# Kernel tuning notes

Hardware: AMD Instinct MI355X
Metric: run time of the kernel (lower is better)

## Reference

```python
import jax, jax.numpy as jnp
import numpy as np

# Config (Qwen3-4B-like, from ModelConfig defaults in source)
B = 32          # batch = number of decode requests = total_q
H = 32          # num_attention_heads
KVH = 8         # num_key_value_heads
G = H // KVH    # num_kv_groups = 4
D = 128         # head_dim
HID = 2560      # hidden_size
PS = 16         # page_size
MAXP = 128      # max_num_pages per request
NPAGES = B * MAXP   # 4096 pages in pool
MAXKV = MAXP * PS   # 2048
THETA = 5000000.0
EPS = 1e-6


def setup_inputs() -> dict:
    key = jax.random.key(0)
    ks = jax.random.split(key, 12)
    x = jax.random.normal(ks[0], (1, B, HID), dtype=jnp.float32)
    Wq = jax.random.normal(ks[1], (H * D, HID), dtype=jnp.float32) * 0.02
    Wk = jax.random.normal(ks[2], (KVH * D, HID), dtype=jnp.float32) * 0.02
    Wv = jax.random.normal(ks[3], (KVH * D, HID), dtype=jnp.float32) * 0.02
    Wo = jax.random.normal(ks[4], (HID, H * D), dtype=jnp.float32) * 0.02
    q_norm_w = jnp.ones((D,), dtype=jnp.float32)
    k_norm_w = jnp.ones((D,), dtype=jnp.float32)
    K_pool = jax.random.normal(ks[5], (NPAGES, PS, KVH, D), dtype=jnp.float32) * 0.02
    V_pool = jax.random.normal(ks[6], (NPAGES, PS, KVH, D), dtype=jnp.float32) * 0.02
    # each request owns a disjoint contiguous run of pages
    page_indices = jnp.arange(NPAGES, dtype=jnp.int32).reshape(B, MAXP)
    # KV length AFTER writing the single new decode token, in [128, MAXKV]
    lengths_after = jax.random.randint(ks[7], (B,), 128, MAXKV + 1).astype(jnp.int32)
    pos = lengths_after - 1                                  # position of new token
    page_of = page_indices[jnp.arange(B), pos // PS]         # page holding it
    slot_mapping = page_of.astype(jnp.int64) * PS + (pos % PS).astype(jnp.int64)
    # RoPE tables at the new-token positions: cos/sin (1, total_q, 1, D)
    inv_freq = 1.0 / (THETA ** (jnp.arange(0, D, 2, dtype=jnp.float32) / D))
    ang = pos.astype(jnp.float32)[:, None] * inv_freq[None, :]   # (B, D/2)
    ang = jnp.concatenate([ang, ang], axis=-1)                   # (B, D)
    cos = jnp.cos(ang)[None, :, None, :]
    sin = jnp.sin(ang)[None, :, None, :]
    return {"x": x, "cos": cos, "sin": sin, "Wq": Wq, "Wk": Wk, "Wv": Wv,
            "Wo": Wo, "q_norm_w": q_norm_w, "k_norm_w": k_norm_w,
            "K_pool": K_pool, "V_pool": V_pool, "page_indices": page_indices,
            "lengths_after": lengths_after, "slot_mapping": slot_mapping}


def _rmsnorm(x, w):
    xf = x.astype(jnp.float32)
    xf = xf * jax.lax.rsqrt(jnp.mean(xf * xf, axis=-1, keepdims=True) + EPS)
    return (w * xf).astype(x.dtype)


def _rope(x, cos, sin):
    # x: (1, heads, S, D); cos/sin: (1, S, 1, D) -> (1, 1, S, D)
    c = jnp.swapaxes(cos, 1, 2).astype(x.dtype)
    s = jnp.swapaxes(sin, 1, 2).astype(x.dtype)
    x1, x2 = jnp.split(x, 2, axis=-1)
    rot = jnp.concatenate([-x2, x1], axis=-1)
    return x * c + rot * s


def reference(x, cos, sin, Wq, Wk, Wv, Wo, q_norm_w, k_norm_w,
              K_pool, V_pool, page_indices, lengths_after, slot_mapping):
    total_q = x.shape[1]  # == B for decode
    # projections -> (1, heads, total_q, D)
    q = jnp.einsum('bsh,oh->bso', x, Wq).reshape(1, total_q, H, D).transpose(0, 2, 1, 3)
    k = jnp.einsum('bsh,oh->bso', x, Wk).reshape(1, total_q, KVH, D).transpose(0, 2, 1, 3)
    v = jnp.einsum('bsh,oh->bso', x, Wv).reshape(1, total_q, KVH, D).transpose(0, 2, 1, 3)
    # QK-norm (per-head RMSNorm on head_dim), then RoPE
    q = _rope(_rmsnorm(q, q_norm_w), cos, sin)
    k = _rope(_rmsnorm(k, k_norm_w), cos, sin)
    # write new K/V into the page pool (index_copy_ equivalent)
    k_pack = jnp.swapaxes(k[0], 0, 1)  # (total_q, KVH, D)
    v_pack = jnp.swapaxes(v[0], 0, 1)
    Kf = K_pool.reshape(NPAGES * PS, KVH, D).at[slot_mapping].set(k_pack)
    Vf = V_pool.reshape(NPAGES * PS, KVH, D).at[slot_mapping].set(v_pack)
    Kp = Kf.reshape(NPAGES, PS, KVH, D)
    Vp = Vf.reshape(NPAGES, PS, KVH, D)
    # decode path: full page-table gather per request
    flat_idx = page_indices.reshape(-1)
    k_all = Kp[flat_idx].reshape(B, MAXKV, KVH, D)
    v_all = Vp[flat_idx].reshape(B, MAXKV, KVH, D)
    # GQA attention, single query per request; scale = 1/sqrt(D) (SDPA default)
    qg = jnp.swapaxes(q[0], 0, 1).reshape(B, KVH, G, D)  # (B, KVH, G, D)
    scores = jnp.einsum('bkgd,bskd->bkgs', qg, k_all) * (1.0 / np.sqrt(D))
    invalid = jnp.arange(MAXKV)[None, :] >= lengths_after[:, None]  # (B, MAXKV)
    scores = jnp.where(invalid[:, None, None, :], -jnp.inf, scores)
    probs = jax.nn.softmax(scores, axis=-1)
    out = jnp.einsum('bkgs,bskd->bkgd', probs, v_all).reshape(B, H * D)
    y = jnp.einsum('bo,ho->bh', out, Wo)  # o_proj
    return y[None]  # (1, total_q, HID)
```

## Files before the change

kernel.cpp:

```cpp
#include <hip/hip_runtime.h>
#include <math.h>

#define NB    32
#define HIDV  2560
#define HD    128
#define NQH   32
#define NKVH  8

typedef __bf16 bf16x8 __attribute__((ext_vector_type(8)));
typedef float  f32x4  __attribute__((ext_vector_type(4)));

__device__ __forceinline__ unsigned bfpack(float a, float b) {
  unsigned ua = __float_as_uint(a), ub = __float_as_uint(b);
  ua = (ua + 0x7FFFu + ((ua >> 16) & 1u)) >> 16;
  ub = (ub + 0x7FFFu + ((ub >> 16) & 1u)) >> 16;
  return ua | (ub << 16);
}

__device__ __forceinline__ void gemm_body(
    const float* __restrict__ X, const float* __restrict__ W,
    float* __restrict__ P, int N, int K, int f0, int kc, int t,
    unsigned short* Wl, unsigned short* Xl) {
  const float* Wg = W + (size_t)f0 * K + (size_t)kc * 256;
  #pragma unroll
  for (int i = 0; i < 16; ++i) {
    int idx = i * 256 + t;
    int row = idx >> 6, c4 = idx & 63;
    float4 w4 = *(const float4*)(Wg + (size_t)row * K + c4 * 4);
    *(uint2*)((char*)Wl + row * 528 + c4 * 8) =
        make_uint2(bfpack(w4.x, w4.y), bfpack(w4.z, w4.w));
  }
  const float* Xg = X + (size_t)kc * 256;
  #pragma unroll
  for (int i = 0; i < 8; ++i) {
    int idx = i * 256 + t;
    int row = idx >> 6, c4 = idx & 63;
    float4 x4 = *(const float4*)(Xg + (size_t)row * K + c4 * 4);
    *(uint2*)((char*)Xl + row * 528 + c4 * 8) =
        make_uint2(bfpack(x4.x, x4.y), bfpack(x4.z, x4.w));
  }
  __syncthreads();

  const int w = t >> 6, l = t & 63;
  const int rA = l & 15, kq = l >> 4;
  f32x4 acc0 = {0.f, 0.f, 0.f, 0.f}, acc1 = {0.f, 0.f, 0.f, 0.f};
  const char* pa0 = (const char*)Xl + rA * 528 + kq * 16;
  const char* pa1 = pa0 + 16 * 528;
  const char* pb  = (const char*)Wl + (w * 16 + rA) * 528 + kq * 16;
  #pragma unroll
  for (int ks = 0; ks < 8; ++ks) {
    bf16x8 a0 = *(const bf16x8*)(pa0 + ks * 64);
    bf16x8 a1 = *(const bf16x8*)(pa1 + ks * 64);
    bf16x8 bb = *(const bf16x8*)(pb  + ks * 64);
    acc0 = __builtin_amdgcn_mfma_f32_16x16x32_bf16(a0, bb, acc0, 0, 0, 0);
    acc1 = __builtin_amdgcn_mfma_f32_16x16x32_bf16(a1, bb, acc1, 0, 0, 0);
  }
  const int fcol = f0 + w * 16 + rA;
  float* Pr = P + ((size_t)kc * 32) * N + fcol;
  #pragma unroll
  for (int j = 0; j < 4; ++j) {
    int b0 = kq * 4 + j;
    Pr[(size_t)b0 * N]        = acc0[j];
    Pr[(size_t)(b0 + 16) * N] = acc1[j];
  }
}

__global__ __launch_bounds__(256) void qkv_gemm(
    const float* __restrict__ X, const float* __restrict__ Wq,
    const float* __restrict__ Wk, const float* __restrict__ Wv,
    float* __restrict__ qp, float* __restrict__ kp, float* __restrict__ vp) {
  __shared__ __align__(16) unsigned short Wl[64 * 264];
  __shared__ __align__(16) unsigned short Xl[32 * 264];
  const int bx = blockIdx.x;
  const float* W; float* P; int N, f0;
  if (bx < 64)      { W = Wq; P = qp; N = 4096; f0 = bx * 64; }
  else if (bx < 80) { W = Wk; P = kp; N = 1024; f0 = (bx - 64) * 64; }
  else              { W = Wv; P = vp; N = 1024; f0 = (bx - 80) * 64; }
  gemm_body(X, W, P, N, 2560, f0, blockIdx.y, threadIdx.x, Wl, Xl);
}

__global__ __launch_bounds__(256) void o_gemm(
    const float* __restrict__ X, const float* __restrict__ W,
    float* __restrict__ P) {
  __shared__ __align__(16) unsigned short Wl[64 * 264];
  __shared__ __align__(16) unsigned short Xl[32 * 264];
  gemm_body(X, W, P, 2560, 4096, blockIdx.x * 64, blockIdx.y, threadIdx.x, Wl, Xl);
}

__global__ __launch_bounds__(128) void finqkv(
    const float* __restrict__ qp, const float* __restrict__ kp,
    const float* __restrict__ vp, const float* __restrict__ cosb,
    const float* __restrict__ sinb, const float* __restrict__ qw,
    const float* __restrict__ kw, float* __restrict__ qn,
    float* __restrict__ kn, float* __restrict__ vn) {
  const int b = blockIdx.x, h = blockIdx.y, d = threadIdx.x;
  float x = 0.f;
  if (h < 32) {
    #pragma unroll
    for (int c = 0; c < 10; ++c) x += qp[(size_t)(c * 32 + b) * 4096 + h * 128 + d];
  } else if (h < 40) {
    #pragma unroll
    for (int c = 0; c < 10; ++c) x += kp[(size_t)(c * 32 + b) * 1024 + (h - 32) * 128 + d];
  } else {
    #pragma unroll
    for (int c = 0; c < 10; ++c) x += vp[(size_t)(c * 32 + b) * 1024 + (h - 40) * 128 + d];
  }
  if (h >= 40) { vn[((size_t)b * 8 + (h - 40)) * 128 + d] = x; return; }

  __shared__ float red[2];
  __shared__ float sh[128];
  float ss = x * x;
  #pragma unroll
  for (int mk = 1; mk < 64; mk <<= 1) ss += __shfl_xor(ss, mk);
  if ((d & 63) == 0) red[d >> 6] = ss;
  __syncthreads();
  const float inv = rsqrtf((red[0] + red[1]) * (1.f / 128.f) + 1e-6f);
  const float* nw = (h < 32) ? qw : kw;
  const float xn = x * inv * nw[d];
  sh[d] = xn;
  __syncthreads();
  const float rot = (d < 64) ? -sh[d + 64] : sh[d - 64];
  const float o = xn * cosb[b * 128 + d] + rot * sinb[b * 128 + d];
  if (h < 32) qn[((size_t)b * 32 + h) * 128 + d] = o;
  else        kn[((size_t)b * 8 + (h - 32)) * 128 + d] = o;
}

__global__ __launch_bounds__(512) void attn(
    const float* __restrict__ Kp, const float* __restrict__ Vp,
    const float* __restrict__ qn, const float* __restrict__ kn,
    const float* __restrict__ vn, const int* __restrict__ pidx,
    const int* __restrict__ lens, float* __restrict__ ao) {
  const int b = blockIdx.x >> 3, kvh = blockIdx.x & 7;
  const int t = threadIdx.x, w = t >> 6, l = t & 63;
  const int sub = l >> 4, di = (l & 15) * 8;
  __shared__ int pages[128];
  __shared__ float mmS[32][4], msS[32][4];
  __shared__ __align__(16) float maccS[32][4][128];
  if (t < 128) pages[t] = pidx[b * 128 + t];
  __syncthreads();
  const int len = lens[b], lim = len - 1;

  float qf[4][8];
  const float SC = 0.08838834764831845f * 1.4426950408889634f;
  #pragma unroll
  for (int g = 0; g < 4; ++g)
    #pragma unroll
    for (int j = 0; j < 8; ++j)
      qf[g][j] = qn[((size_t)b * 32 + kvh * 4 + g) * 128 + di + j] * SC;

  float m[4], se[4], acc[4][8];
  #pragma unroll
  for (int g = 0; g < 4; ++g) {
    m[g] = -INFINITY; se[g] = 0.f;
    #pragma unroll
    for (int j = 0; j < 8; ++j) acc[g][j] = 0.f;
  }

  const int t0 = w * 4 + sub;
  const int nit = (lim + 31) >> 5;

  auto update = [&](const float (&ck)[8], const float (&cv)[8], bool valid) {
    float s[4];
    #pragma unroll
    for (int g = 0; g < 4; ++g) {
      float d8 = 0.f;
      #pragma unroll
      for (int j = 0; j < 8; ++j) d8 += qf[g][j] * ck[j];
      s[g] = d8;
    }
    #pragma unroll
    for (int mk = 1; mk < 16; mk <<= 1) {
      #pragma unroll
      for (int g = 0; g < 4; ++g) s[g] += __shfl_xor(s[g], mk);
    }
    if (valid) {
      #pragma unroll
      for (int g = 0; g < 4; ++g) {
        const float sg = s[g];
        if (sg > m[g]) {
          const float scf = exp2f(m[g] - sg);
          m[g] = sg;
          se[g] = se[g] * scf + 1.f;
          #pragma unroll
          for (int j = 0; j < 8; ++j) acc[g][j] = acc[g][j] * scf + cv[j];
        } else {
          const float p = exp2f(sg - m[g]);
          se[g] += p;
          #pragma unroll
          for (int j = 0; j < 8; ++j) acc[g][j] += p * cv[j];
        }
      }
    }
  };

  f32x4 ka0, ka1, va0, va1, kb0, kb1, vb0, vb1;
  {
    int tt = min(t0, lim - 1);
    size_t a = ((size_t)pages[tt >> 4] * 16 + (tt & 15)) * 1024 + kvh * 128 + di;
    ka0 = *(const f32x4*)(Kp + a); ka1 = *(const f32x4*)(Kp + a + 4);
    va0 = *(const f32x4*)(Vp + a); va1 = *(const f32x4*)(Vp + a + 4);
  }
  if (nit > 1) {
    int tt = min(32 + t0, lim - 1);
    size_t a = ((size_t)pages[tt >> 4] * 16 + (tt & 15)) * 1024 + kvh * 128 + di;
    kb0 = *(const f32x4*)(Kp + a); kb1 = *(const f32x4*)(Kp + a + 4);
    vb0 = *(const f32x4*)(Vp + a); vb1 = *(const f32x4*)(Vp + a + 4);
  }
  for (int it = 0; it < nit; it += 2) {
    {
      const float ck[8] = {ka0[0], ka0[1], ka0[2], ka0[3], ka1[0], ka1[1], ka1[2], ka1[3]};
      const float cv[8] = {va0[0], va0[1], va0[2], va0[3], va1[0], va1[1], va1[2], va1[3]};
      if (it + 2 < nit) {
        int tt = min((it + 2) * 32 + t0, lim - 1);
        size_t a = ((size_t)pages[tt >> 4] * 16 + (tt & 15)) * 1024 + kvh * 128 + di;
        ka0 = *(const f32x4*)(Kp + a); ka1 = *(const f32x4*)(Kp + a + 4);
        va0 = *(const f32x4*)(Vp + a); va1 = *(const f32x4*)(Vp + a + 4);
      }
      update(ck, cv, it * 32 + t0 < lim);
    }
    if (it + 1 < nit) {
      const float ck[8] = {kb0[0], kb0[1], kb0[2], kb0[3], kb1[0], kb1[1], kb1[2], kb1[3]};
      const float cv[8] = {vb0[0], vb0[1], vb0[2], vb0[3], vb1[0], vb1[1], vb1[2], vb1[3]};
      if (it + 3 < nit) {
        int tt = min((it + 3) * 32 + t0, lim - 1);
        size_t a = ((size_t)pages[tt >> 4] * 16 + (tt & 15)) * 1024 + kvh * 128 + di;
        kb0 = *(const f32x4*)(Kp + a); kb1 = *(const f32x4*)(Kp + a + 4);
        vb0 = *(const f32x4*)(Vp + a); vb1 = *(const f32x4*)(Vp + a + 4);
      }
      update(ck, cv, (it + 1) * 32 + t0 < lim);
    }
  }

  if (w == 0) {
    const float* kr = kn + ((size_t)b * 8 + kvh) * 128 + di;
    const float* vr = vn + ((size_t)b * 8 + kvh) * 128 + di;
    float ck[8], cv[8];
    #pragma unroll
    for (int j = 0; j < 8; ++j) { ck[j] = kr[j]; cv[j] = vr[j]; }
    update(ck, cv, sub == 0);
  }

  const int st = w * 4 + sub;
  if ((l & 15) == 0) {
    #pragma unroll
    for (int g = 0; g < 4; ++g) { mmS[st][g] = m[g]; msS[st][g] = se[g]; }
  }
  #pragma unroll
  for (int g = 0; g < 4; ++g)
    #pragma unroll
    for (int j = 0; j < 8; ++j) maccS[st][g][di + j] = acc[g][j];
  __syncthreads();

  const int g = t >> 7, dd = t & 127;
  float M = -INFINITY;
  #pragma unroll
  for (int s2 = 0; s2 < 32; ++s2) M = fmaxf(M, mmS[s2][g]);
  float den = 0.f, num = 0.f;
  for (int s2 = 0; s2 < 32; ++s2) {
    const float wg = exp2f(mmS[s2][g] - M);
    den += wg * msS[s2][g];
    num += wg * maccS[s2][g][dd];
  }
  ao[((size_t)b * 32 + kvh * 4 + g) * 128 + dd] = num / den;
}

__global__ __launch_bounds__(256) void oreduce(const float* __restrict__ op,
                                               float* __restrict__ y) {
  const int i = blockIdx.x * 256 + threadIdx.x;
  float s = 0.f;
  #pragma unroll
  for (int c = 0; c < 16; ++c) s += op[(size_t)c * (32 * 2560) + i];
  y[i] = s;
}

extern "C" void kernel_launch(void* const* d_in, const int* in_sizes, int n_in,
                              void* d_out, int out_size, void* d_ws, size_t ws_size,
                              hipStream_t stream) {
  const float* x    = (const float*)d_in[0];
  const float* cosb = (const float*)d_in[1];
  const float* sinb = (const float*)d_in[2];
  const float* Wq   = (const float*)d_in[3];
  const float* Wk   = (const float*)d_in[4];
  const float* Wv   = (const float*)d_in[5];
  const float* Wo   = (const float*)d_in[6];
  const float* qw   = (const float*)d_in[7];
  const float* kw   = (const float*)d_in[8];
  const float* Kp   = (const float*)d_in[9];
  const float* Vp   = (const float*)d_in[10];
  const int*   pidx = (const int*)d_in[11];
  const int*   lens = (const int*)d_in[12];
  float* y = (float*)d_out;

  float* ws = (float*)d_ws;
  float* qp = ws;
  float* kp = qp + 1310720;
  float* vp = kp + 327680;
  float* qn = vp + 327680;
  float* kn = qn + 131072;
  float* vn = kn + 32768;
  float* ao = vn + 32768;
  float* op = qp;
  (void)in_sizes; (void)n_in; (void)out_size; (void)ws_size;

  qkv_gemm<<<dim3(96, 10), 256, 0, stream>>>(x, Wq, Wk, Wv, qp, kp, vp);
  finqkv<<<dim3(32, 48), 128, 0, stream>>>(qp, kp, vp, cosb, sinb, qw, kw, qn, kn, vn);
  attn<<<256, 512, 0, stream>>>(Kp, Vp, qn, kn, vn, pidx, lens, ao);
  o_gemm<<<dim3(40, 16), 256, 0, stream>>>(ao, Wo, op);
  oreduce<<<320, 256, 0, stream>>>(op, y);
}
```

Measured before the change: 99.00 us.

## Drop split-K in projection GEMMs and deepen attention KV prefetch

The QKV and output-projection GEMMs now loop over all K slabs inside one block instead of splitting K across the grid. This removes the partial-sum buffers, the separate oreduce kernel and the 10-way summation in finqkv. The attention loop now keeps four KV tiles in flight instead of two, to hide more load latency. In exchange the GEMM grids shrink to 96 and 40 blocks, far fewer than the number of CUs. Each block also streams its weight slabs serially with a barrier between them, so weight-bandwidth utilization may drop sharply.

```diff
diff --git a/kernel.cpp b/kernel.cpp
--- a/kernel.cpp
+++ b/kernel.cpp
@@ -19,44 +19,48 @@
 
 __device__ __forceinline__ void gemm_body(
     const float* __restrict__ X, const float* __restrict__ W,
-    float* __restrict__ P, int N, int K, int f0, int kc, int t,
+    float* __restrict__ P, int N, int K, int f0, int slabs, int t,
     unsigned short* Wl, unsigned short* Xl) {
-  const float* Wg = W + (size_t)f0 * K + (size_t)kc * 256;
-  #pragma unroll
-  for (int i = 0; i < 16; ++i) {
-    int idx = i * 256 + t;
-    int row = idx >> 6, c4 = idx & 63;
-    float4 w4 = *(const float4*)(Wg + (size_t)row * K + c4 * 4);
-    *(uint2*)((char*)Wl + row * 528 + c4 * 8) =
-        make_uint2(bfpack(w4.x, w4.y), bfpack(w4.z, w4.w));
-  }
-  const float* Xg = X + (size_t)kc * 256;
-  #pragma unroll
-  for (int i = 0; i < 8; ++i) {
-    int idx = i * 256 + t;
-    int row = idx >> 6, c4 = idx & 63;
-    float4 x4 = *(const float4*)(Xg + (size_t)row * K + c4 * 4);
-    *(uint2*)((char*)Xl + row * 528 + c4 * 8) =
-        make_uint2(bfpack(x4.x, x4.y), bfpack(x4.z, x4.w));
-  }
-  __syncthreads();
-
   const int w = t >> 6, l = t & 63;
   const int rA = l & 15, kq = l >> 4;
   f32x4 acc0 = {0.f, 0.f, 0.f, 0.f}, acc1 = {0.f, 0.f, 0.f, 0.f};
-  const char* pa0 = (const char*)Xl + rA * 528 + kq * 16;
-  const char* pa1 = pa0 + 16 * 528;
-  const char* pb  = (const char*)Wl + (w * 16 + rA) * 528 + kq * 16;
-  #pragma unroll
-  for (int ks = 0; ks < 8; ++ks) {
-    bf16x8 a0 = *(const bf16x8*)(pa0 + ks * 64);
-    bf16x8 a1 = *(const bf16x8*)(pa1 + ks * 64);
-    bf16x8 bb = *(const bf16x8*)(pb  + ks * 64);
-    acc0 = __builtin_amdgcn_mfma_f32_16x16x32_bf16(a0, bb, acc0, 0, 0, 0);
-    acc1 = __builtin_amdgcn_mfma_f32_16x16x32_bf16(a1, bb, acc1, 0, 0, 0);
+
+  for (int s = 0; s < slabs; ++s) {
+    if (s) __syncthreads();
+    const float* Wg = W + (size_t)f0 * K + (size_t)s * 256;
+    #pragma unroll
+    for (int i = 0; i < 16; ++i) {
+      int idx = i * 256 + t;
+      int row = idx >> 6, c4 = idx & 63;
+      float4 w4 = *(const float4*)(Wg + (size_t)row * K + c4 * 4);
+      *(uint2*)((char*)Wl + row * 528 + c4 * 8) =
+          make_uint2(bfpack(w4.x, w4.y), bfpack(w4.z, w4.w));
+    }
+    const float* Xg = X + (size_t)s * 256;
+    #pragma unroll
+    for (int i = 0; i < 8; ++i) {
+      int idx = i * 256 + t;
+      int row = idx >> 6, c4 = idx & 63;
+      float4 x4 = *(const float4*)(Xg + (size_t)row * K + c4 * 4);
+      *(uint2*)((char*)Xl + row * 528 + c4 * 8) =
+          make_uint2(bfpack(x4.x, x4.y), bfpack(x4.z, x4.w));
+    }
+    __syncthreads();
+
+    const char* pa0 = (const char*)Xl + rA * 528 + kq * 16;
+    const char* pa1 = pa0 + 16 * 528;
+    const char* pb  = (const char*)Wl + (w * 16 + rA) * 528 + kq * 16;
+    #pragma unroll
+    for (int ks = 0; ks < 8; ++ks) {
+      bf16x8 a0 = *(const bf16x8*)(pa0 + ks * 64);
+      bf16x8 a1 = *(const bf16x8*)(pa1 + ks * 64);
+      bf16x8 bb = *(const bf16x8*)(pb  + ks * 64);
+      acc0 = __builtin_amdgcn_mfma_f32_16x16x32_bf16(a0, bb, acc0, 0, 0, 0);
+      acc1 = __builtin_amdgcn_mfma_f32_16x16x32_bf16(a1, bb, acc1, 0, 0, 0);
+    }
   }
   const int fcol = f0 + w * 16 + rA;
-  float* Pr = P + ((size_t)kc * 32) * N + fcol;
+  float* Pr = P + fcol;
   #pragma unroll
   for (int j = 0; j < 4; ++j) {
     int b0 = kq * 4 + j;
@@ -76,15 +80,15 @@
   if (bx < 64)      { W = Wq; P = qp; N = 4096; f0 = bx * 64; }
   else if (bx < 80) { W = Wk; P = kp; N = 1024; f0 = (bx - 64) * 64; }
   else              { W = Wv; P = vp; N = 1024; f0 = (bx - 80) * 64; }
-  gemm_body(X, W, P, N, 2560, f0, blockIdx.y, threadIdx.x, Wl, Xl);
+  gemm_body(X, W, P, N, 2560, f0, 10, threadIdx.x, Wl, Xl);
 }
 
 __global__ __launch_bounds__(256) void o_gemm(
     const float* __restrict__ X, const float* __restrict__ W,
-    float* __restrict__ P) {
+    float* __restrict__ y) {
   __shared__ __align__(16) unsigned short Wl[64 * 264];
   __shared__ __align__(16) unsigned short Xl[32 * 264];
-  gemm_body(X, W, P, 2560, 4096, blockIdx.x * 64, blockIdx.y, threadIdx.x, Wl, Xl);
+  gemm_body(X, W, y, 2560, 4096, blockIdx.x * 64, 16, threadIdx.x, Wl, Xl);
 }
 
 __global__ __launch_bounds__(128) void finqkv(
@@ -94,17 +98,10 @@
     const float* __restrict__ kw, float* __restrict__ qn,
     float* __restrict__ kn, float* __restrict__ vn) {
   const int b = blockIdx.x, h = blockIdx.y, d = threadIdx.x;
-  float x = 0.f;
-  if (h < 32) {
-    #pragma unroll
-    for (int c = 0; c < 10; ++c) x += qp[(size_t)(c * 32 + b) * 4096 + h * 128 + d];
-  } else if (h < 40) {
-    #pragma unroll
-    for (int c = 0; c < 10; ++c) x += kp[(size_t)(c * 32 + b) * 1024 + (h - 32) * 128 + d];
-  } else {
-    #pragma unroll
-    for (int c = 0; c < 10; ++c) x += vp[(size_t)(c * 32 + b) * 1024 + (h - 40) * 128 + d];
-  }
+  float x;
+  if (h < 32)      x = qp[(size_t)b * 4096 + h * 128 + d];
+  else if (h < 40) x = kp[(size_t)b * 1024 + (h - 32) * 128 + d];
+  else             x = vp[(size_t)b * 1024 + (h - 40) * 128 + d];
   if (h >= 40) { vn[((size_t)b * 8 + (h - 40)) * 128 + d] = x; return; }
 
   __shared__ float red[2];
@@ -193,43 +190,41 @@
     }
   };
 
-  f32x4 ka0, ka1, va0, va1, kb0, kb1, vb0, vb1;
-  {
-    int tt = min(t0, lim - 1);
-    size_t a = ((size_t)pages[tt >> 4] * 16 + (tt & 15)) * 1024 + kvh * 128 + di;
-    ka0 = *(const f32x4*)(Kp + a); ka1 = *(const f32x4*)(Kp + a + 4);
-    va0 = *(const f32x4*)(Vp + a); va1 = *(const f32x4*)(Vp + a + 4);
-  }
-  if (nit > 1) {
-    int tt = min(32 + t0, lim - 1);
-    size_t a = ((size_t)pages[tt >> 4] * 16 + (tt & 15)) * 1024 + kvh * 128 + di;
-    kb0 = *(const f32x4*)(Kp + a); kb1 = *(const f32x4*)(Kp + a + 4);
-    vb0 = *(const f32x4*)(Vp + a); vb1 = *(const f32x4*)(Vp + a + 4);
-  }
-  for (int it = 0; it < nit; it += 2) {
-    {
-      const float ck[8] = {ka0[0], ka0[1], ka0[2], ka0[3], ka1[0], ka1[1], ka1[2], ka1[3]};
-      const float cv[8] = {va0[0], va0[1], va0[2], va0[3], va1[0], va1[1], va1[2], va1[3]};
-      if (it + 2 < nit) {
-        int tt = min((it + 2) * 32 + t0, lim - 1);
-        size_t a = ((size_t)pages[tt >> 4] * 16 + (tt & 15)) * 1024 + kvh * 128 + di;
-        ka0 = *(const f32x4*)(Kp + a); ka1 = *(const f32x4*)(Kp + a + 4);
-        va0 = *(const f32x4*)(Vp + a); va1 = *(const f32x4*)(Vp + a + 4);
-      }
-      update(ck, cv, it * 32 + t0 < lim);
-    }
-    if (it + 1 < nit) {
-      const float ck[8] = {kb0[0], kb0[1], kb0[2], kb0[3], kb1[0], kb1[1], kb1[2], kb1[3]};
-      const float cv[8] = {vb0[0], vb0[1], vb0[2], vb0[3], vb1[0], vb1[1], vb1[2], vb1[3]};
-      if (it + 3 < nit) {
-        int tt = min((it + 3) * 32 + t0, lim - 1);
-        size_t a = ((size_t)pages[tt >> 4] * 16 + (tt & 15)) * 1024 + kvh * 128 + di;
-        kb0 = *(const f32x4*)(Kp + a); kb1 = *(const f32x4*)(Kp + a + 4);
-        vb0 = *(const f32x4*)(Vp + a); vb1 = *(const f32x4*)(Vp + a + 4);
-      }
-      update(ck, cv, (it + 1) * 32 + t0 < lim);
-    }
-  }
+#define LOAD_ST(K0, K1, V0, V1, TOK) do {                                     \
+    int tt = min((TOK), lim - 1);                                             \
+    size_t a = ((size_t)pages[tt >> 4] * 16 + (tt & 15)) * 1024               \
+               + kvh * 128 + di;                                              \
+    K0 = *(const f32x4*)(Kp + a); K1 = *(const f32x4*)(Kp + a + 4);           \
+    V0 = *(const f32x4*)(Vp + a); V1 = *(const f32x4*)(Vp + a + 4);           \
+  } while (0)
+
+#define CONSUME(K0, K1, V0, V1, IT, PF_K0, PF_K1, PF_V0, PF_V1, PFIT) {       \
+    const float ck[8] = {K0[0], K0[1], K0[2], K0[3],                          \
+                         K1[0], K1[1], K1[2], K1[3]};                         \
+    const float cv[8] = {V0[0], V0[1], V0[2], V0[3],                          \
+                         V1[0], V1[1], V1[2], V1[3]};                         \
+    if ((PFIT) < nit) LOAD_ST(PF_K0, PF_K1, PF_V0, PF_V1, (PFIT) * 32 + t0);  \
+    update(ck, cv, (IT) * 32 + t0 < lim);                                     \
+  }
+
+  f32x4 kA0, kA1, vA0, vA1, kB0, kB1, vB0, vB1;
+  f32x4 kC0, kC1, vC0, vC1, kD0, kD1, vD0, vD1;
+  LOAD_ST(kA0, kA1, vA0, vA1, t0);
+  if (nit > 1) LOAD_ST(kB0, kB1, vB0, vB1, 32 + t0);
+  if (nit > 2) LOAD_ST(kC0, kC1, vC0, vC1, 64 + t0);
+  if (nit > 3) LOAD_ST(kD0, kD1, vD0, vD1, 96 + t0);
+
+  for (int it = 0; it < nit; it += 4) {
+    CONSUME(kA0, kA1, vA0, vA1, it, kA0, kA1, vA0, vA1, it + 4);
+    if (it + 1 < nit)
+      CONSUME(kB0, kB1, vB0, vB1, it + 1, kB0, kB1, vB0, vB1, it + 5);
+    if (it + 2 < nit)
+      CONSUME(kC0, kC1, vC0, vC1, it + 2, kC0, kC1, vC0, vC1, it + 6);
+    if (it + 3 < nit)
+      CONSUME(kD0, kD1, vD0, vD1, it + 3, kD0, kD1, vD0, vD1, it + 7);
+  }
+#undef CONSUME
+#undef LOAD_ST
 
   if (w == 0) {
     const float* kr = kn + ((size_t)b * 8 + kvh) * 128 + di;
@@ -262,15 +257,6 @@
     num += wg * maccS[s2][g][dd];
   }
   ao[((size_t)b * 32 + kvh * 4 + g) * 128 + dd] = num / den;
-}
-
-__global__ __launch_bounds__(256) void oreduce(const float* __restrict__ op,
-                                               float* __restrict__ y) {
-  const int i = blockIdx.x * 256 + threadIdx.x;
-  float s = 0.f;
-  #pragma unroll
-  for (int c = 0; c < 16; ++c) s += op[(size_t)c * (32 * 2560) + i];
-  y[i] = s;
 }
 
 extern "C" void kernel_launch(void* const* d_in, const int* in_sizes, int n_in,
@@ -293,18 +279,16 @@
 
   float* ws = (float*)d_ws;
   float* qp = ws;
-  float* kp = qp + 1310720;
-  float* vp = kp + 327680;
-  float* qn = vp + 327680;
+  float* kp = qp + 131072;
+  float* vp = kp + 32768;
+  float* qn = vp + 32768;
   float* kn = qn + 131072;
   float* vn = kn + 32768;
   float* ao = vn + 32768;
-  float* op = qp;
   (void)in_sizes; (void)n_in; (void)out_size; (void)ws_size;
 
-  qkv_gemm<<<dim3(96, 10), 256, 0, stream>>>(x, Wq, Wk, Wv, qp, kp, vp);
+  qkv_gemm<<<96, 256, 0, stream>>>(x, Wq, Wk, Wv, qp, kp, vp);
   finqkv<<<dim3(32, 48), 128, 0, stream>>>(qp, kp, vp, cosb, sinb, qw, kw, qn, kn, vn);
   attn<<<256, 512, 0, stream>>>(Kp, Vp, qn, kn, vn, pidx, lens, ao);
-  o_gemm<<<dim3(40, 16), 256, 0, stream>>>(ao, Wo, op);
-  oreduce<<<320, 256, 0, stream>>>(op, y);
-}
+  o_gemm<<<40, 256, 0, stream>>>(ao, Wo, y);
+}
```

After: 137.9 us. 39.3% more time.
